# Kernel tuning notes

Hardware: AMD Instinct MI355X
Metric: run time of the kernel (lower is better)

Reference implementation:

```python
import jax, jax.numpy as jnp
import numpy as np

N, E = 100000, 1600000
NF, HC, NC = 32, 64, 64


def setup_inputs() -> dict:
    key = jax.random.key(0)
    ks = jax.random.split(key, 12)
    s = 0.05
    return {
        "x": jax.random.normal(ks[0], (N, NF), dtype=jnp.float32),
        "edge_index": jax.random.randint(ks[1], (2, E), 0, N, dtype=jnp.int64),
        "eps1": jnp.float32(0.0),
        "eps2": jnp.float32(0.0),
        "W1a": jax.random.normal(ks[2], (NF, HC), dtype=jnp.float32) * s,
        "b1a": jnp.zeros((HC,), dtype=jnp.float32),
        "W1b": jax.random.normal(ks[3], (HC, HC), dtype=jnp.float32) * s,
        "b1b": jnp.zeros((HC,), dtype=jnp.float32),
        "W2a": jax.random.normal(ks[4], (HC, HC), dtype=jnp.float32) * s,
        "b2a": jnp.zeros((HC,), dtype=jnp.float32),
        "W2b": jax.random.normal(ks[5], (HC, NC), dtype=jnp.float32) * s,
        "b2b": jnp.zeros((NC,), dtype=jnp.float32),
    }


def _gin_conv(h, src, dst, eps, Wa, ba, Wb, bb, num_nodes):
    # sum-aggregate neighbor features: out[dst] += h[src]
    agg = jax.ops.segment_sum(h[src], dst, num_segments=num_nodes)
    z = (1.0 + eps) * h + agg
    # 2-layer MLP: Linear -> ReLU -> Linear
    z = jax.nn.relu(z @ Wa + ba)
    return z @ Wb + bb


def reference(x, edge_index, eps1, eps2, W1a, b1a, W1b, b1b, W2a, b2a, W2b, b2b):
    src, dst = edge_index[0], edge_index[1]
    n = x.shape[0]
    emb = _gin_conv(x, src, dst, eps1, W1a, b1a, W1b, b1b, n)  # [N, HC]
    h = jax.nn.relu(emb)  # dropout is identity in eval mode
    logits = _gin_conv(h, src, dst, eps2, W2a, b2a, W2b, b2b, n)  # [N, NC]
    return (logits, emb)
```

## Files before the change

kernel.cpp:

```cpp
#include <hip/hip_runtime.h>


#define NFEAT 32
#define HID   64
#define NCLS  64

#define BSH   9
#define BNODES 512
#define NBKT_MAX 256
#define BCAP  16384

typedef unsigned int uint;
typedef unsigned short ushortT;
typedef __attribute__((ext_vector_type(8))) short bf16x8;
typedef __attribute__((ext_vector_type(4))) float f32x4;

__device__ __forceinline__ int clampi(int v, int hi){ v = v < 0 ? 0 : v; return v > hi ? hi : v; }

__device__ __forceinline__ ushortT f2b(float f){
  uint u = __float_as_uint(f);
  u = (u + 0x7FFFu + ((u >> 16) & 1u)) >> 16;
  return (ushortT)u;
}
__device__ __forceinline__ float b2f_lo(uint u){ return __uint_as_float(u << 16); }
__device__ __forceinline__ float b2f_hi(uint u){ return __uint_as_float(u & 0xFFFF0000u); }
__device__ __forceinline__ uint pack2(float lo, float hi){
  return (uint)f2b(lo) | ((uint)f2b(hi) << 16);
}


__global__ void k_bucket(const int* __restrict__ src, const int* __restrict__ dst,
                         int E, int N, int nbkt,
                         int* __restrict__ bktCnt, int* __restrict__ bktData){
  __shared__ int s_cnt[NBKT_MAX];
  __shared__ int s_base[NBKT_MAX];
  const int t = threadIdx.x;
  for (int j = t; j < nbkt; j += 256) s_cnt[j] = 0;
  __syncthreads();

  const int e0 = blockIdx.x * 4096;
  const int e1 = min(e0 + 4096, E);
  for (int e = e0 + t; e < e1; e += 256){
    int d = clampi(dst[e], N-1);
    atomicAdd(&s_cnt[d >> BSH], 1);
  }
  __syncthreads();
  for (int j = t; j < nbkt; j += 256){
    int c = s_cnt[j];
    s_base[j] = (c > 0) ? atomicAdd(&bktCnt[j], c) : 0;
    s_cnt[j] = 0;
  }
  __syncthreads();
  for (int e = e0 + t; e < e1; e += 256){
    int d = clampi(dst[e], N-1);
    int s = clampi(src[e], N-1);
    int b = d >> BSH;
    int p = s_base[b] + atomicAdd(&s_cnt[b], 1);
    if (p < BCAP)
      bktData[(size_t)b * BCAP + p] = ((d & (BNODES-1)) << 17) | s;
  }
}


__global__ void k_bktscan(const int* __restrict__ bktCnt, int nbkt,
                          int* __restrict__ bktBase, int* __restrict__ rowptr, int N){
  __shared__ int s[NBKT_MAX];
  const int t = threadIdx.x;
  int v = (t < nbkt) ? min(bktCnt[t], BCAP) : 0;
  s[t] = v;
  __syncthreads();
  for (int off = 1; off < NBKT_MAX; off <<= 1){
    int add = (t >= off) ? s[t-off] : 0;
    __syncthreads();
    s[t] += add;
    __syncthreads();
  }
  if (t < nbkt) bktBase[t] = s[t] - v;
  if (t == nbkt-1){ bktBase[nbkt] = s[t]; rowptr[N] = s[t]; }
}


__global__ __launch_bounds__(BNODES)
void k_build(const int* __restrict__ bktCnt, const int* __restrict__ bktBase,
             const int* __restrict__ bktData,
             int* __restrict__ rowptr, int* __restrict__ eidx, int N){
  __shared__ int s_h[BNODES];
  __shared__ int s_cur[BNODES];
  const int b = blockIdx.x, t = threadIdx.x;
  const int cnt  = min(bktCnt[b], BCAP);
  const int base = bktBase[b];
  const int* __restrict__ data = bktData + (size_t)b * BCAP;

  s_h[t] = 0;
  __syncthreads();
  for (int e = t; e < cnt; e += BNODES) atomicAdd(&s_h[data[e] >> 17], 1);
  __syncthreads();

  int deg = s_h[t];
  for (int off = 1; off < BNODES; off <<= 1){
    int add = (t >= off) ? s_h[t-off] : 0;
    __syncthreads();
    s_h[t] += add;
    __syncthreads();
  }
  int excl = s_h[t] - deg;
  int node = b * BNODES + t;
  if (node < N) rowptr[node] = base + excl;
  s_cur[t] = excl;
  __syncthreads();

  for (int e = t; e < cnt; e += BNODES){
    int val = data[e];
    int d = val >> 17;
    int p = atomicAdd(&s_cur[d], 1);
    eidx[base + p] = val & 0x1FFFF;
  }
}


__global__ void k_cvt(const float* __restrict__ in, ushortT* __restrict__ out, int n4){
  int t = blockIdx.x*blockDim.x + threadIdx.x;
  if (t >= n4) return;
  float4 v = reinterpret_cast<const float4*>(in)[t];
  ushort4 o = { f2b(v.x), f2b(v.y), f2b(v.z), f2b(v.w) };
  reinterpret_cast<ushort4*>(out)[t] = o;
}


__global__ void k_wprep(const float* __restrict__ W1a, const float* __restrict__ W1b,
                        const float* __restrict__ W2a, const float* __restrict__ W2b,
                        ushortT* __restrict__ T1a, ushortT* __restrict__ T1b,
                        ushortT* __restrict__ T2a, ushortT* __restrict__ T2b){
  int t = blockIdx.x*256 + threadIdx.x;
  const float* W; ushortT* T; int K; int base;
  if      (t <  2048){ W=W1a; T=T1a; K=32; base=0;     }
  else if (t <  6144){ W=W1b; T=T1b; K=64; base=2048;  }
  else if (t < 10240){ W=W2a; T=T2a; K=64; base=6144;  }
  else if (t < 14336){ W=W2b; T=T2b; K=64; base=10240; }
  else return;
  int o = t - base;
  int k = o >> 6, c = o & 63;
  T[c*K + k] = f2b(W[o]);
}


template<int K, bool WRITE_HB>
__global__ __launch_bounds__(256)
void k_fused(const uint4* __restrict__ f4,
             const int* __restrict__ rowptr, const int* __restrict__ eidx,
             const float* __restrict__ epsP,
             const ushortT* __restrict__ WaT,
             const float* __restrict__ ba,
             const ushortT* __restrict__ WbT,
             const float* __restrict__ bb,
             float* __restrict__ out,
             ushortT* __restrict__ hb, int N){
  constexpr int RS = K/8;
  constexpr int CH = K/32;
  __shared__ __align__(16) ushortT zt[64*K];
  __shared__ __align__(16) ushortT ht[64*64];
  const int t = threadIdx.x;
  const int row0 = blockIdx.x * 64;

  {
    const int li = t >> 2, q = t & 3;
    const int node = row0 + li;
    float acc[CH][8];
    #pragma unroll
    for (int c = 0; c < CH; ++c)
      #pragma unroll
      for (int j = 0; j < 8; ++j) acc[c][j] = 0.f;

    if (node < N){
      const float se = 1.0f + epsP[0];
      int b = rowptr[node], e = rowptr[node+1];
      for (; b + 1 < e; b += 2){
        int s0 = eidx[b], s1 = eidx[b+1];
        #pragma unroll
        for (int c = 0; c < CH; ++c){
          uint4 v = f4[(size_t)s0*RS + q*CH + c];
          uint4 u = f4[(size_t)s1*RS + q*CH + c];
          acc[c][0] += b2f_lo(v.x) + b2f_lo(u.x);
          acc[c][1] += b2f_hi(v.x) + b2f_hi(u.x);
          acc[c][2] += b2f_lo(v.y) + b2f_lo(u.y);
          acc[c][3] += b2f_hi(v.y) + b2f_hi(u.y);
          acc[c][4] += b2f_lo(v.z) + b2f_lo(u.z);
          acc[c][5] += b2f_hi(v.z) + b2f_hi(u.z);
          acc[c][6] += b2f_lo(v.w) + b2f_lo(u.w);
          acc[c][7] += b2f_hi(v.w) + b2f_hi(u.w);
        }
      }
      if (b < e){
        int s0 = eidx[b];
        #pragma unroll
        for (int c = 0; c < CH; ++c){
          uint4 v = f4[(size_t)s0*RS + q*CH + c];
          acc[c][0] += b2f_lo(v.x); acc[c][1] += b2f_hi(v.x);
          acc[c][2] += b2f_lo(v.y); acc[c][3] += b2f_hi(v.y);
          acc[c][4] += b2f_lo(v.z); acc[c][5] += b2f_hi(v.z);
          acc[c][6] += b2f_lo(v.w); acc[c][7] += b2f_hi(v.w);
        }
      }
      #pragma unroll
      for (int c = 0; c < CH; ++c){
        uint4 v = f4[(size_t)node*RS + q*CH + c];
        acc[c][0] = fmaf(se, b2f_lo(v.x), acc[c][0]);
        acc[c][1] = fmaf(se, b2f_hi(v.x), acc[c][1]);
        acc[c][2] = fmaf(se, b2f_lo(v.y), acc[c][2]);
        acc[c][3] = fmaf(se, b2f_hi(v.y), acc[c][3]);
        acc[c][4] = fmaf(se, b2f_lo(v.z), acc[c][4]);
        acc[c][5] = fmaf(se, b2f_hi(v.z), acc[c][5]);
        acc[c][6] = fmaf(se, b2f_lo(v.w), acc[c][6]);
        acc[c][7] = fmaf(se, b2f_hi(v.w), acc[c][7]);
      }
    }
    #pragma unroll
    for (int c = 0; c < CH; ++c){
      uint4 z;
      z.x = pack2(acc[c][0], acc[c][1]);
      z.y = pack2(acc[c][2], acc[c][3]);
      z.z = pack2(acc[c][4], acc[c][5]);
      z.w = pack2(acc[c][6], acc[c][7]);
      reinterpret_cast<uint4*>(zt)[li*RS + q*CH + c] = z;
    }
  }
  __syncthreads();

  const int w  = t >> 6, l = t & 63;
  const int lr = l & 15;
  const int lg = l >> 4;
  f32x4 c1[4];
  #pragma unroll
  for (int c = 0; c < 4; ++c){ float bv = ba[c*16 + lr]; c1[c] = (f32x4){bv,bv,bv,bv}; }
  #pragma unroll
  for (int kf = 0; kf < K/32; ++kf){
    bf16x8 a = *reinterpret_cast<const bf16x8*>(&zt[(w*16 + lr)*K + kf*32 + lg*8]);
    #pragma unroll
    for (int c = 0; c < 4; ++c){
      bf16x8 bfr = *reinterpret_cast<const bf16x8*>(&WaT[(c*16 + lr)*K + kf*32 + lg*8]);
      c1[c] = __builtin_amdgcn_mfma_f32_16x16x32_bf16(a, bfr, c1[c], 0, 0, 0);
    }
  }
  #pragma unroll
  for (int c = 0; c < 4; ++c)
    #pragma unroll
    for (int r = 0; r < 4; ++r)
      ht[(w*16 + lg*4 + r)*64 + c*16 + lr] = f2b(fmaxf(c1[c][r], 0.f));
  __syncthreads();

  f32x4 c2[4];
  #pragma unroll
  for (int c = 0; c < 4; ++c){ float bv = bb[c*16 + lr]; c2[c] = (f32x4){bv,bv,bv,bv}; }
  #pragma unroll
  for (int kf = 0; kf < 2; ++kf){
    bf16x8 a = *reinterpret_cast<const bf16x8*>(&ht[(w*16 + lr)*64 + kf*32 + lg*8]);
    #pragma unroll
    for (int c = 0; c < 4; ++c){
      bf16x8 bfr = *reinterpret_cast<const bf16x8*>(&WbT[(c*16 + lr)*64 + kf*32 + lg*8]);
      c2[c] = __builtin_amdgcn_mfma_f32_16x16x32_bf16(a, bfr, c2[c], 0, 0, 0);
    }
  }
  #pragma unroll
  for (int c = 0; c < 4; ++c)
    #pragma unroll
    for (int r = 0; r < 4; ++r){
      int row = row0 + w*16 + lg*4 + r;
      if (row < N){
        float v = c2[c][r];
        out[(size_t)row*64 + c*16 + lr] = v;
        if (WRITE_HB) hb[(size_t)row*64 + c*16 + lr] = f2b(fmaxf(v, 0.f));
      }
    }
}


extern "C" void kernel_launch(void* const* d_in, const int* in_sizes, int n_in,
                              void* d_out, int out_size, void* d_ws, size_t ws_size,
                              hipStream_t stream) {
  const int N = in_sizes[0] / NFEAT;
  const int E = in_sizes[1] / 2;
  const int nbkt = (N + BNODES - 1) / BNODES;

  const float* x    = (const float*)d_in[0];
  const int*   ei   = (const int*)d_in[1];
  const int*   srcI = ei;
  const int*   dstI = ei + E;
  const float* eps1 = (const float*)d_in[2];
  const float* eps2 = (const float*)d_in[3];
  const float* W1a  = (const float*)d_in[4];
  const float* b1a  = (const float*)d_in[5];
  const float* W1b  = (const float*)d_in[6];
  const float* b1b  = (const float*)d_in[7];
  const float* W2a  = (const float*)d_in[8];
  const float* b2a  = (const float*)d_in[9];
  const float* W2b  = (const float*)d_in[10];
  const float* b2b  = (const float*)d_in[11];

  float* outLogits = (float*)d_out;
  float* outEmb    = outLogits + (size_t)N * HID;

  char* w = (char*)d_ws;
  size_t off = 0;
  auto alloc = [&](size_t bytes) -> void* {
    void* p = w + off;
    off = (off + bytes + 255) & ~(size_t)255;
    return p;
  };
  int*     rowptr  = (int*)alloc((size_t)(N+1) * sizeof(int));
  int*     eidx    = (int*)alloc((size_t)E * sizeof(int));
  int*     bktCnt  = (int*)alloc((size_t)NBKT_MAX * sizeof(int));
  int*     bktBase = (int*)alloc((size_t)(NBKT_MAX+1) * sizeof(int));
  ushortT* T1a     = (ushortT*)alloc(64*32*sizeof(ushortT));
  ushortT* T1b     = (ushortT*)alloc(64*64*sizeof(ushortT));
  ushortT* T2a     = (ushortT*)alloc(64*64*sizeof(ushortT));
  ushortT* T2b     = (ushortT*)alloc(64*64*sizeof(ushortT));
  int*     bktData = (int*)alloc((size_t)NBKT_MAX * BCAP * sizeof(int));
  ushortT* xb      = (ushortT*)bktData;
  ushortT* hb      = (ushortT*)alloc((size_t)N * HID * sizeof(ushortT));

  hipMemsetAsync(bktCnt, 0, (size_t)NBKT_MAX * sizeof(int), stream);
  k_bucket <<<(E+4095)/4096, 256, 0, stream>>>(srcI, dstI, E, N, nbkt, bktCnt, bktData);
  k_bktscan<<<1, NBKT_MAX, 0, stream>>>(bktCnt, nbkt, bktBase, rowptr, N);
  k_build  <<<nbkt, BNODES, 0, stream>>>(bktCnt, bktBase, bktData, rowptr, eidx, N);

  k_cvt  <<<((N*NFEAT/4)+255)/256, 256, 0, stream>>>(x, xb, N*NFEAT/4);
  k_wprep<<<56, 256, 0, stream>>>(W1a, W1b, W2a, W2b, T1a, T1b, T2a, T2b);

  const int nblk = (N + 63) / 64;
  k_fused<NFEAT, true><<<nblk, 256, 0, stream>>>((const uint4*)xb, rowptr, eidx,
      eps1, T1a, b1a, T1b, b1b, outEmb, hb, N);

  k_fused<HID, false><<<nblk, 256, 0, stream>>>((const uint4*)hb, rowptr, eidx,
      eps2, T2a, b2a, T2b, b2b, outLogits, (ushortT*)nullptr, N);
}
```

Measured before the change: 142.7 us.

## Split fused GIN aggregation across two edge lanes per node with LDS-staged indices

The fused GIN kernel now uses 512 threads per block. Each node gets 8 threads, and two lane groups handle alternating edges, with partial sums combined by an xor shuffle. The block's edge-index range is staged into shared memory, and each gather loop is unrolled to issue several independent row loads. The MLP MFMA stage is spread across 8 waves, each computing 2 output column tiles instead of 4. The aim is more memory-level parallelism in the gather, traded for higher register and LDS pressure per block and a fallback to global loads when a block has more than ECAP edges.

```diff
diff --git a/kernel.cpp b/kernel.cpp
--- a/kernel.cpp
+++ b/kernel.cpp
@@ -9,6 +9,7 @@
 #define BNODES 512
 #define NBKT_MAX 256
 #define BCAP  16384
+#define ECAP  2048
 
 typedef unsigned int uint;
 typedef unsigned short ushortT;
@@ -145,7 +146,7 @@
 
 
 template<int K, bool WRITE_HB>
-__global__ __launch_bounds__(256)
+__global__ __launch_bounds__(512)
 void k_fused(const uint4* __restrict__ f4,
              const int* __restrict__ rowptr, const int* __restrict__ eidx,
              const float* __restrict__ epsP,
@@ -156,119 +157,149 @@
              float* __restrict__ out,
              ushortT* __restrict__ hb, int N){
   constexpr int RS = K/8;
-  constexpr int CH = K/32;
+  constexpr int CH = RS/4;
+  constexpr int U  = (CH == 1) ? 4 : 2;
+  __shared__ int s_row[65];
+  __shared__ int s_eidx[ECAP];
   __shared__ __align__(16) ushortT zt[64*K];
   __shared__ __align__(16) ushortT ht[64*64];
   const int t = threadIdx.x;
   const int row0 = blockIdx.x * 64;
 
+  const int e0 = rowptr[min(row0, N)];
+  const int e1 = rowptr[min(row0 + 64, N)];
+  if (t < 65){
+    int idx = row0 + t; if (idx > N) idx = N;
+    s_row[t] = rowptr[idx];
+  }
+  const int cnt = e1 - e0;
+  for (int j = t; j < cnt && j < ECAP; j += 512) s_eidx[j] = eidx[e0 + j];
+  __syncthreads();
+
   {
-    const int li = t >> 2, q = t & 3;
-    const int node = row0 + li;
-    float acc[CH][8];
-    #pragma unroll
-    for (int c = 0; c < CH; ++c)
-      #pragma unroll
-      for (int j = 0; j < 8; ++j) acc[c][j] = 0.f;
-
-    if (node < N){
-      const float se = 1.0f + epsP[0];
-      int b = rowptr[node], e = rowptr[node+1];
-      for (; b + 1 < e; b += 2){
-        int s0 = eidx[b], s1 = eidx[b+1];
+    const int n = t >> 3;
+    const int L = t & 7;
+    const int q = L & (RS/CH - 1);
+    const int s = L >> 2;
+    const int node = row0 + n;
+    float acc[CH*8];
+    #pragma unroll
+    for (int j = 0; j < CH*8; ++j) acc[j] = 0.f;
+
+    const int b = s_row[n] - e0;
+    const int e = s_row[n+1] - e0;
+    int i = b + s;
+    for (; i + 2*(U-1) < e; i += 2*U){
+      int src[U];
+      #pragma unroll
+      for (int u = 0; u < U; ++u){
+        int ii = i + 2*u;
+        src[u] = (ii < ECAP) ? s_eidx[ii] : eidx[e0 + ii];
+      }
+      uint4 v[U][CH];
+      #pragma unroll
+      for (int u = 0; u < U; ++u)
+        #pragma unroll
+        for (int c = 0; c < CH; ++c)
+          v[u][c] = f4[(size_t)src[u]*RS + q*CH + c];
+      #pragma unroll
+      for (int u = 0; u < U; ++u)
         #pragma unroll
         for (int c = 0; c < CH; ++c){
-          uint4 v = f4[(size_t)s0*RS + q*CH + c];
-          uint4 u = f4[(size_t)s1*RS + q*CH + c];
-          acc[c][0] += b2f_lo(v.x) + b2f_lo(u.x);
-          acc[c][1] += b2f_hi(v.x) + b2f_hi(u.x);
-          acc[c][2] += b2f_lo(v.y) + b2f_lo(u.y);
-          acc[c][3] += b2f_hi(v.y) + b2f_hi(u.y);
-          acc[c][4] += b2f_lo(v.z) + b2f_lo(u.z);
-          acc[c][5] += b2f_hi(v.z) + b2f_hi(u.z);
-          acc[c][6] += b2f_lo(v.w) + b2f_lo(u.w);
-          acc[c][7] += b2f_hi(v.w) + b2f_hi(u.w);
+          acc[c*8+0] += b2f_lo(v[u][c].x); acc[c*8+1] += b2f_hi(v[u][c].x);
+          acc[c*8+2] += b2f_lo(v[u][c].y); acc[c*8+3] += b2f_hi(v[u][c].y);
+          acc[c*8+4] += b2f_lo(v[u][c].z); acc[c*8+5] += b2f_hi(v[u][c].z);
+          acc[c*8+6] += b2f_lo(v[u][c].w); acc[c*8+7] += b2f_hi(v[u][c].w);
         }
-      }
-      if (b < e){
-        int s0 = eidx[b];
-        #pragma unroll
-        for (int c = 0; c < CH; ++c){
-          uint4 v = f4[(size_t)s0*RS + q*CH + c];
-          acc[c][0] += b2f_lo(v.x); acc[c][1] += b2f_hi(v.x);
-          acc[c][2] += b2f_lo(v.y); acc[c][3] += b2f_hi(v.y);
-          acc[c][4] += b2f_lo(v.z); acc[c][5] += b2f_hi(v.z);
-          acc[c][6] += b2f_lo(v.w); acc[c][7] += b2f_hi(v.w);
-        }
-      }
+    }
+    for (; i < e; i += 2){
+      int src0 = (i < ECAP) ? s_eidx[i] : eidx[e0 + i];
+      #pragma unroll
+      for (int c = 0; c < CH; ++c){
+        uint4 v = f4[(size_t)src0*RS + q*CH + c];
+        acc[c*8+0] += b2f_lo(v.x); acc[c*8+1] += b2f_hi(v.x);
+        acc[c*8+2] += b2f_lo(v.y); acc[c*8+3] += b2f_hi(v.y);
+        acc[c*8+4] += b2f_lo(v.z); acc[c*8+5] += b2f_hi(v.z);
+        acc[c*8+6] += b2f_lo(v.w); acc[c*8+7] += b2f_hi(v.w);
+      }
+    }
+    if (s == 1 && node < N){
+      const float se = 1.0f + epsP[0];
       #pragma unroll
       for (int c = 0; c < CH; ++c){
         uint4 v = f4[(size_t)node*RS + q*CH + c];
-        acc[c][0] = fmaf(se, b2f_lo(v.x), acc[c][0]);
-        acc[c][1] = fmaf(se, b2f_hi(v.x), acc[c][1]);
-        acc[c][2] = fmaf(se, b2f_lo(v.y), acc[c][2]);
-        acc[c][3] = fmaf(se, b2f_hi(v.y), acc[c][3]);
-        acc[c][4] = fmaf(se, b2f_lo(v.z), acc[c][4]);
-        acc[c][5] = fmaf(se, b2f_hi(v.z), acc[c][5]);
-        acc[c][6] = fmaf(se, b2f_lo(v.w), acc[c][6]);
-        acc[c][7] = fmaf(se, b2f_hi(v.w), acc[c][7]);
-      }
-    }
-    #pragma unroll
-    for (int c = 0; c < CH; ++c){
-      uint4 z;
-      z.x = pack2(acc[c][0], acc[c][1]);
-      z.y = pack2(acc[c][2], acc[c][3]);
-      z.z = pack2(acc[c][4], acc[c][5]);
-      z.w = pack2(acc[c][6], acc[c][7]);
-      reinterpret_cast<uint4*>(zt)[li*RS + q*CH + c] = z;
-    }
-  }
-  __syncthreads();
-
-  const int w  = t >> 6, l = t & 63;
+        acc[c*8+0] = fmaf(se, b2f_lo(v.x), acc[c*8+0]);
+        acc[c*8+1] = fmaf(se, b2f_hi(v.x), acc[c*8+1]);
+        acc[c*8+2] = fmaf(se, b2f_lo(v.y), acc[c*8+2]);
+        acc[c*8+3] = fmaf(se, b2f_hi(v.y), acc[c*8+3]);
+        acc[c*8+4] = fmaf(se, b2f_lo(v.z), acc[c*8+4]);
+        acc[c*8+5] = fmaf(se, b2f_hi(v.z), acc[c*8+5]);
+        acc[c*8+6] = fmaf(se, b2f_lo(v.w), acc[c*8+6]);
+        acc[c*8+7] = fmaf(se, b2f_hi(v.w), acc[c*8+7]);
+      }
+    }
+    #pragma unroll
+    for (int j = 0; j < CH*8; ++j) acc[j] += __shfl_xor(acc[j], 4);
+    if (s == 0){
+      #pragma unroll
+      for (int c = 0; c < CH; ++c){
+        uint4 z;
+        z.x = pack2(acc[c*8+0], acc[c*8+1]);
+        z.y = pack2(acc[c*8+2], acc[c*8+3]);
+        z.z = pack2(acc[c*8+4], acc[c*8+5]);
+        z.w = pack2(acc[c*8+6], acc[c*8+7]);
+        reinterpret_cast<uint4*>(zt)[n*RS + q*CH + c] = z;
+      }
+    }
+  }
+  __syncthreads();
+
+  const int w  = t >> 6;
+  const int l  = t & 63;
   const int lr = l & 15;
   const int lg = l >> 4;
-  f32x4 c1[4];
-  #pragma unroll
-  for (int c = 0; c < 4; ++c){ float bv = ba[c*16 + lr]; c1[c] = (f32x4){bv,bv,bv,bv}; }
+  const int rf = w & 3;
+  const int c0 = (w >> 2) * 2;
+  f32x4 c1[2];
+  #pragma unroll
+  for (int cl = 0; cl < 2; ++cl){ float bv = ba[(c0+cl)*16 + lr]; c1[cl] = (f32x4){bv,bv,bv,bv}; }
   #pragma unroll
   for (int kf = 0; kf < K/32; ++kf){
-    bf16x8 a = *reinterpret_cast<const bf16x8*>(&zt[(w*16 + lr)*K + kf*32 + lg*8]);
-    #pragma unroll
-    for (int c = 0; c < 4; ++c){
-      bf16x8 bfr = *reinterpret_cast<const bf16x8*>(&WaT[(c*16 + lr)*K + kf*32 + lg*8]);
-      c1[c] = __builtin_amdgcn_mfma_f32_16x16x32_bf16(a, bfr, c1[c], 0, 0, 0);
-    }
-  }
-  #pragma unroll
-  for (int c = 0; c < 4; ++c)
+    bf16x8 a = *reinterpret_cast<const bf16x8*>(&zt[(rf*16 + lr)*K + kf*32 + lg*8]);
+    #pragma unroll
+    for (int cl = 0; cl < 2; ++cl){
+      bf16x8 bfr = *reinterpret_cast<const bf16x8*>(&WaT[((c0+cl)*16 + lr)*K + kf*32 + lg*8]);
+      c1[cl] = __builtin_amdgcn_mfma_f32_16x16x32_bf16(a, bfr, c1[cl], 0, 0, 0);
+    }
+  }
+  #pragma unroll
+  for (int cl = 0; cl < 2; ++cl)
     #pragma unroll
     for (int r = 0; r < 4; ++r)
-      ht[(w*16 + lg*4 + r)*64 + c*16 + lr] = f2b(fmaxf(c1[c][r], 0.f));
-  __syncthreads();
-
-  f32x4 c2[4];
-  #pragma unroll
-  for (int c = 0; c < 4; ++c){ float bv = bb[c*16 + lr]; c2[c] = (f32x4){bv,bv,bv,bv}; }
+      ht[(rf*16 + lg*4 + r)*64 + (c0+cl)*16 + lr] = f2b(fmaxf(c1[cl][r], 0.f));
+  __syncthreads();
+
+  f32x4 c2[2];
+  #pragma unroll
+  for (int cl = 0; cl < 2; ++cl){ float bv = bb[(c0+cl)*16 + lr]; c2[cl] = (f32x4){bv,bv,bv,bv}; }
   #pragma unroll
   for (int kf = 0; kf < 2; ++kf){
-    bf16x8 a = *reinterpret_cast<const bf16x8*>(&ht[(w*16 + lr)*64 + kf*32 + lg*8]);
-    #pragma unroll
-    for (int c = 0; c < 4; ++c){
-      bf16x8 bfr = *reinterpret_cast<const bf16x8*>(&WbT[(c*16 + lr)*64 + kf*32 + lg*8]);
-      c2[c] = __builtin_amdgcn_mfma_f32_16x16x32_bf16(a, bfr, c2[c], 0, 0, 0);
-    }
-  }
-  #pragma unroll
-  for (int c = 0; c < 4; ++c)
+    bf16x8 a = *reinterpret_cast<const bf16x8*>(&ht[(rf*16 + lr)*64 + kf*32 + lg*8]);
+    #pragma unroll
+    for (int cl = 0; cl < 2; ++cl){
+      bf16x8 bfr = *reinterpret_cast<const bf16x8*>(&WbT[((c0+cl)*16 + lr)*64 + kf*32 + lg*8]);
+      c2[cl] = __builtin_amdgcn_mfma_f32_16x16x32_bf16(a, bfr, c2[cl], 0, 0, 0);
+    }
+  }
+  #pragma unroll
+  for (int cl = 0; cl < 2; ++cl)
     #pragma unroll
     for (int r = 0; r < 4; ++r){
-      int row = row0 + w*16 + lg*4 + r;
+      int row = row0 + rf*16 + lg*4 + r;
       if (row < N){
-        float v = c2[c][r];
-        out[(size_t)row*64 + c*16 + lr] = v;
-        if (WRITE_HB) hb[(size_t)row*64 + c*16 + lr] = f2b(fmaxf(v, 0.f));
+        float v = c2[cl][r];
+        out[(size_t)row*64 + (c0+cl)*16 + lr] = v;
+        if (WRITE_HB) hb[(size_t)row*64 + (c0+cl)*16 + lr] = f2b(fmaxf(v, 0.f));
       }
     }
 }
@@ -327,9 +358,9 @@
   k_wprep<<<56, 256, 0, stream>>>(W1a, W1b, W2a, W2b, T1a, T1b, T2a, T2b);
 
   const int nblk = (N + 63) / 64;
-  k_fused<NFEAT, true><<<nblk, 256, 0, stream>>>((const uint4*)xb, rowptr, eidx,
+  k_fused<NFEAT, true><<<nblk, 512, 0, stream>>>((const uint4*)xb, rowptr, eidx,
       eps1, T1a, b1a, T1b, b1b, outEmb, hb, N);
 
-  k_fused<HID, false><<<nblk, 256, 0, stream>>>((const uint4*)hb, rowptr, eidx,
+  k_fused<HID, false><<<nblk, 512, 0, stream>>>((const uint4*)hb, rowptr, eidx,
       eps2, T2a, b2a, T2b, b2b, outLogits, (ushortT*)nullptr, N);
 }
```

After: 133.1 us. -6.7%, faster.
